# Optimization experiments

Hardware: AMD Instinct MI355X
Metric: run time of the kernel (lower is better)

## Reference

```python
import jax, jax.numpy as jnp
import numpy as np

D = 1024
E = 8
K = 2
NUM_ITER = 2
DT = 0.1
H = 64           # controller_hidden
CTX = 2 * D


def _gelu(t):
    return jax.nn.gelu(t, approximate=False)


def _inl(ctrl, x, v, mu):
    # ctrl: [T, 3D] -> alpha, beta, gate chunks of size D
    alpha_raw, beta_raw, gate_raw = jnp.split(ctrl, 3, axis=-1)
    alpha = jax.nn.sigmoid(alpha_raw)
    beta = jax.nn.softplus(beta_raw)
    gate = jax.nn.sigmoid(gate_raw)
    error = x - mu
    v_next = alpha * v - beta * error
    x_next = x + DT * gate * v_next
    return x_next, v_next


def setup_inputs() -> dict:
    key = jax.random.key(0)
    ks = jax.random.split(key, 20)
    s = 0.02
    inp = {
        'x': jax.random.normal(ks[0], (4, 4096, D), jnp.float32),
        # router MLP
        'w_r1': jax.random.normal(ks[1], (D, D // 4), jnp.float32) * s,
        'b_r1': jnp.zeros((D // 4,), jnp.float32),
        'w_r2': jax.random.normal(ks[2], (D // 4, E), jnp.float32) * s,
        'b_r2': jnp.zeros((E,), jnp.float32),
        # halt gate MLP
        'w_h1': jax.random.normal(ks[3], (D, D // 4), jnp.float32) * s,
        'b_h1': jnp.zeros((D // 4,), jnp.float32),
        'w_h2': jax.random.normal(ks[4], (D // 4, 1), jnp.float32) * s,
        'b_h2': jnp.zeros((1,), jnp.float32),
        # expert tables
        'expert_w1': jax.random.normal(ks[5], (E, CTX, H), jnp.float32) * s,
        'expert_b1': jnp.zeros((E, H), jnp.float32),
        'expert_w2': jax.random.normal(ks[6], (E, H, 3 * D), jnp.float32) * s,
        'expert_b2': jnp.zeros((E, 3 * D), jnp.float32),
        # shared expert
        'w_s1': jax.random.normal(ks[7], (CTX, H), jnp.float32) * s,
        'b_s1': jnp.zeros((H,), jnp.float32),
        'w_s2': jax.random.normal(ks[8], (H, 3 * D), jnp.float32) * s,
        'b_s2': jnp.zeros((3 * D,), jnp.float32),
        'shared_weight': jnp.asarray(0.5, jnp.float32),
        # refine MLP
        'w_f1': jax.random.normal(ks[9], (D, 2 * D), jnp.float32) * s,
        'b_f1': jnp.zeros((2 * D,), jnp.float32),
        'w_f2': jax.random.normal(ks[10], (2 * D, D), jnp.float32) * s,
        'b_f2': jnp.zeros((D,), jnp.float32),
        'integration_weight': jnp.full((D,), 0.5, jnp.float32),
        'mu': jnp.zeros((D,), jnp.float32),
    }
    return inp


def reference(x, w_r1, b_r1, w_r2, b_r2, w_h1, b_h1, w_h2, b_h2,
              expert_w1, expert_b1, expert_w2, expert_b2,
              w_s1, b_s1, w_s2, b_s2, shared_weight,
              w_f1, b_f1, w_f2, b_f2, integration_weight, mu):
    B, N, Dm = x.shape
    xf = x.reshape(B * N, Dm)                       # [T, D]

    # router: top-k over softmax probs, renormalized
    logits = _gelu(xf @ w_r1 + b_r1) @ w_r2 + b_r2  # [T, E]
    probs = jax.nn.softmax(logits, axis=-1)
    top_p, top_i = jax.lax.top_k(probs, K)          # [T, K]
    top_p = top_p / jnp.sum(top_p, axis=-1, keepdims=True)

    flat_idx = top_i.reshape(-1)                    # [T*K]
    flat_w = top_p.reshape(-1, 1)                   # [T*K, 1]

    v = jnp.zeros_like(xf)
    integrated = xf
    for _ in range(NUM_ITER):
        ctx = jnp.concatenate([integrated, v], axis=-1)     # [T, 2D]

        # shared expert path
        shared_ctrl = _gelu(ctx @ w_s1 + b_s1) @ w_s2 + b_s2
        x_shared, v_shared = _inl(shared_ctrl, integrated, v, mu)
        sw = jax.nn.sigmoid(shared_weight)

        # routed experts: gather per-token weights, per-token matvec
        ctx_e = jnp.repeat(ctx, K, axis=0)                  # [T*K, 2D]
        x_e = jnp.repeat(integrated, K, axis=0)
        v_e = jnp.repeat(v, K, axis=0)
        w1 = expert_w1[flat_idx]                            # [T*K, 2D, H]
        b1 = expert_b1[flat_idx]
        w2 = expert_w2[flat_idx]                            # [T*K, H, 3D]
        b2 = expert_b2[flat_idx]
        hidden = _gelu(jnp.einsum('tc,tch->th', ctx_e, w1) + b1)
        ctrl = jnp.einsum('th,tho->to', hidden, w2) + b2    # [T*K, 3D]
        x_r, v_r = _inl(ctrl, x_e, v_e, mu)
        x_r = (x_r * flat_w).reshape(B * N, K, Dm).sum(axis=1)
        v_r = (v_r * flat_w).reshape(B * N, K, Dm).sum(axis=1)

        x_next = sw * x_shared + (1.0 - sw) * x_r
        v_next = sw * v_shared + (1.0 - sw) * v_r

        halt = jax.nn.sigmoid(_gelu(x_next @ w_h1 + b_h1) @ w_h2 + b_h2)  # [T,1]
        refined = _gelu(x_next @ w_f1 + b_f1) @ w_f2 + b_f2               # [T,D]
        integrated = integrated + halt * refined * integration_weight
        v = v_next

    return integrated.reshape(B, N, Dm)
```

## Files before the change

### kernel.cpp

```cpp
#include <hip/hip_runtime.h>


#define TOK   16384
#define DDIM  1024
#define NEXP  8
#define DTC   0.1f
#define NDESC 320
#define GPAD  20480

using f32x4 = __attribute__((ext_vector_type(4))) float;
using bfv8  = __attribute__((ext_vector_type(8))) short;

__device__ __forceinline__ unsigned short f2bf(float x){
  unsigned u = __builtin_bit_cast(unsigned, x);
  u += 0x7fffu + ((u >> 16) & 1u);
  return (unsigned short)(u >> 16);
}
__device__ __forceinline__ float bf2f(unsigned short h){
  return __builtin_bit_cast(float, ((unsigned)h) << 16);
}
__device__ __forceinline__ float sigmf(float x){ return 1.0f/(1.0f+__expf(-x)); }
__device__ __forceinline__ float geluf(float x){
  float u = 1.595769122f * __builtin_fmaf(0.044715f*x*x, x, x);
  return x * sigmf(u);
}
__device__ __forceinline__ float softpf(float x){
  return fmaxf(x, 0.0f) + __logf(1.0f + __expf(-fabsf(x)));
}
__device__ __forceinline__ f32x4 mfma16(bfv8 a, bfv8 b, f32x4 c){
  return __builtin_amdgcn_mfma_f32_16x16x32_bf16(a, b, c, 0, 0, 0);
}
typedef __attribute__((address_space(1))) const void gvoid_t;
typedef __attribute__((address_space(3))) void svoid_t;
__device__ __forceinline__ void gload16(const void* g, void* l){
  __builtin_amdgcn_global_load_lds((gvoid_t*)g, (svoid_t*)l, 16, 0, 0);
}

__global__ __launch_bounds__(256) void transpose_cast(
    const float* __restrict__ src, unsigned short* __restrict__ dst, int R, int C)
{
  __shared__ float tile[32][33];
  size_t bo = (size_t)blockIdx.z * R * C;
  const float* s = src + bo;
  unsigned short* d = dst + bo;
  int c0 = blockIdx.x * 32, r0 = blockIdx.y * 32;
  int tx = threadIdx.x, ty = threadIdx.y;
  #pragma unroll
  for (int j = 0; j < 4; j++)
    tile[ty + 8*j][tx] = s[(size_t)(r0 + ty + 8*j) * C + c0 + tx];
  __syncthreads();
  #pragma unroll
  for (int j = 0; j < 4; j++)
    d[(size_t)(c0 + ty + 8*j) * R + r0 + tx] = f2bf(tile[tx][ty + 8*j]);
}

__global__ __launch_bounds__(256) void xinit_k(
    const float* __restrict__ xf, unsigned short* __restrict__ xb)
{
  const int n = TOK * 256;
  for (int i = blockIdx.x * 256 + threadIdx.x; i < n; i += gridDim.x * 256) {
    float4 f = ((const float4*)xf)[i];
    ushort4 u = {f2bf(f.x), f2bf(f.y), f2bf(f.z), f2bf(f.w)};
    ((ushort4*)xb)[i] = u;
  }
}

__global__ __launch_bounds__(256) void ctxb_k(
    const float* __restrict__ xf, const int* __restrict__ tokmap,
    unsigned short* __restrict__ ctx)
{
  const int g = blockIdx.x, tid = threadIdx.x;
  const int t = tokmap[g];
  if (tid < 128) {
    uint4 o4 = {0,0,0,0};
    if (t >= 0) {
      const float4* s = (const float4*)(xf + (size_t)t * 1024) + tid * 2;
      float4 f0 = s[0], f1 = s[1];
      unsigned short tmp[8] = {f2bf(f0.x), f2bf(f0.y), f2bf(f0.z), f2bf(f0.w),
                               f2bf(f1.x), f2bf(f1.y), f2bf(f1.z), f2bf(f1.w)};
      o4 = *(uint4*)tmp;
    }
    *(uint4*)&ctx[(size_t)g * 2048 + tid * 8] = o4;
  } else {
    *(uint4*)&ctx[(size_t)g * 2048 + 1024 + (tid - 128) * 8] = uint4{0,0,0,0};
  }
}

template<int EPI>
__global__ __launch_bounds__(256) void gemm_k(
    const unsigned short* __restrict__ A, int lda,
    const unsigned short* __restrict__ BT,
    const float* __restrict__ bias, const float* __restrict__ bias2,
    int Kd, int N,
    unsigned short* __restrict__ obf, unsigned short* __restrict__ obf2,
    const float* __restrict__ halt, const float* __restrict__ iw,
    float* __restrict__ integ, unsigned short* __restrict__ ctxX,
    const int* __restrict__ pf)
{
  __shared__ unsigned short As[128][64];
  __shared__ unsigned short Bs[128][64];
  const int total = gridDim.x * gridDim.y;
  const int bid = blockIdx.y * gridDim.x + blockIdx.x;
  const int swz = (bid & 7) * (total >> 3) + (bid >> 3);
  const int bx = swz % gridDim.x, by = swz / gridDim.x;

  const int tid  = threadIdx.x, lane = tid & 63, w = tid >> 6;
  const int wm   = w >> 1, wn = w & 1;
  const int gm0  = by * 128, gn0 = bx * 128;
  const int r8   = lane >> 3;
  const int sseg = (lane & 7) ^ r8;

  const unsigned short* aga[4];
  const unsigned short* bga[4];
  #pragma unroll
  for (int c = 0; c < 4; c++) {
    aga[c] = A  + (size_t)(gm0 + w*32 + c*8 + r8) * lda + sseg*8;
    bga[c] = BT + (size_t)(gn0 + w*32 + c*8 + r8) * Kd  + sseg*8;
  }

  f32x4 acc[4][4];
  #pragma unroll
  for (int i = 0; i < 4; i++)
    #pragma unroll
    for (int j = 0; j < 4; j++)
      acc[i][j] = f32x4{0.f,0.f,0.f,0.f};

  const int xr = (lane & 7) << 3;
  for (int k0 = 0; k0 < Kd; k0 += 64) {
    #pragma unroll
    for (int c = 0; c < 4; c++) gload16(aga[c] + k0, &As[w*32 + c*8][0]);
    #pragma unroll
    for (int c = 0; c < 4; c++) gload16(bga[c] + k0, &Bs[w*32 + c*8][0]);
    __syncthreads();
    #pragma unroll
    for (int kk = 0; kk < 64; kk += 32) {
      const int kof = kk + ((lane >> 4) << 3);
      bfv8 a[4], b[4];
      #pragma unroll
      for (int mf = 0; mf < 4; mf++)
        a[mf] = *(const bfv8*)&As[wm*64 + mf*16 + (lane & 15)][kof ^ xr];
      #pragma unroll
      for (int nf = 0; nf < 4; nf++)
        b[nf] = *(const bfv8*)&Bs[wn*64 + nf*16 + (lane & 15)][kof ^ xr];
      #pragma unroll
      for (int mf = 0; mf < 4; mf++)
        #pragma unroll
        for (int nf = 0; nf < 4; nf++)
          acc[mf][nf] = mfma16(a[mf], b[nf], acc[mf][nf]);
    }
    __syncthreads();
  }

  #pragma unroll
  for (int mf = 0; mf < 4; mf++) {
    #pragma unroll
    for (int nf = 0; nf < 4; nf++) {
      int col = gn0 + wn*64 + nf*16 + (lane & 15);
      float bc;
      if (EPI == 2) bc = (col < 2048) ? bias[col] : bias2[col - 2048];
      else          bc = bias[col];
      #pragma unroll
      for (int r = 0; r < 4; r++) {
        int row = gm0 + wm*64 + mf*16 + ((lane >> 4) << 2) + r;
        float v = acc[mf][nf][r] + bc;
        if (EPI == 0) {
          obf[(size_t)row * N + col] = f2bf(geluf(v));
        } else if (EPI == 2) {
          if (col < 2048) obf [(size_t)row * 2048 + col]         = f2bf(geluf(v));
          else            obf2[(size_t)row * 256 + (col - 2048)] = f2bf(geluf(v));
        } else {
          size_t ix = (size_t)row * DDIM + col;
          float nv = integ[ix] + halt[row] * v * iw[col];
          integ[ix] = nv;
          if (ctxX) ctxX[(size_t)pf[row] * 2048 + col] = f2bf(nv);
        }
      }
    }
  }
}

__global__ __launch_bounds__(256) void router_k(
    const unsigned short* __restrict__ h1, const float* __restrict__ w_r2,
    const float* __restrict__ b_r2, int* __restrict__ topi, float* __restrict__ topw)
{
  int t = blockIdx.x * 4 + (threadIdx.x >> 6);
  int lane = threadIdx.x & 63;
  const unsigned short* hp = h1 + (size_t)t * 256 + lane * 4;
  float hv[4];
  #pragma unroll
  for (int j = 0; j < 4; j++) hv[j] = bf2f(hp[j]);
  float acc[8];
  #pragma unroll
  for (int e = 0; e < 8; e++) acc[e] = 0.f;
  #pragma unroll
  for (int j = 0; j < 4; j++) {
    const float* wr = w_r2 + (size_t)(lane*4 + j) * 8;
    #pragma unroll
    for (int e = 0; e < 8; e++) acc[e] += hv[j] * wr[e];
  }
  #pragma unroll
  for (int off = 32; off > 0; off >>= 1)
    #pragma unroll
    for (int e = 0; e < 8; e++) acc[e] += __shfl_xor(acc[e], off);
  if (lane == 0) {
    float lg[8];
    #pragma unroll
    for (int e = 0; e < 8; e++) lg[e] = acc[e] + b_r2[e];
    int i0 = 0; float m0 = lg[0];
    #pragma unroll
    for (int e = 1; e < 8; e++) if (lg[e] > m0) { m0 = lg[e]; i0 = e; }
    int i1 = -1; float m1 = -3.4e38f;
    #pragma unroll
    for (int e = 0; e < 8; e++) if (e != i0 && lg[e] > m1) { m1 = lg[e]; i1 = e; }
    float w0 = 1.0f / (1.0f + expf(m1 - m0));
    topi[t*2] = i0; topi[t*2+1] = i1;
    topw[t*2] = w0; topw[t*2+1] = 1.0f - w0;
  }
}

__global__ __launch_bounds__(256) void haltgate_k(
    const unsigned short* __restrict__ h1, const float* __restrict__ w_h2,
    const float* __restrict__ b_h2, float* __restrict__ halt)
{
  int t = blockIdx.x * 4 + (threadIdx.x >> 6);
  int lane = threadIdx.x & 63;
  const unsigned short* hp = h1 + (size_t)t * 256 + lane * 4;
  float s = 0.f;
  #pragma unroll
  for (int j = 0; j < 4; j++) s += bf2f(hp[j]) * w_h2[lane*4 + j];
  #pragma unroll
  for (int off = 32; off > 0; off >>= 1) s += __shfl_xor(s, off);
  if (lane == 0) halt[t] = sigmf(s + b_h2[0]);
}

__global__ __launch_bounds__(256) void pairb_k(
    const int* __restrict__ topi, const float* __restrict__ topw,
    int* __restrict__ cnt, int* __restrict__ plist, float* __restrict__ wA)
{
  int t = blockIdx.x * 256 + threadIdx.x;
  int a = topi[2*t], b = topi[2*t+1];
  float wa = topw[2*t];
  if (a > b) { int tmp = a; a = b; b = tmp; wa = 1.0f - wa; }
  int pid = a * 8 + b;
  int pos = atomicAdd(&cnt[pid], 1);
  plist[pid * TOK + pos] = t;
  wA[t] = wa;
}

__global__ void desc_k(const int* __restrict__ cnt, int4* __restrict__ desc,
                       int* __restrict__ ndesc, int* __restrict__ pbase)
{
  if (threadIdx.x == 0 && blockIdx.x == 0) {
    int nt = 0, rb = 0;
    for (int p = 0; p < 64; p++) {
      pbase[p] = rb;
      int c = cnt[p];
      for (int o = 0; o < c; o += 64) {
        int rem = c - o; if (rem > 64) rem = 64;
        desc[nt] = make_int4(p, rb + o, rem, 0);
        nt++;
      }
      rb += (c + 63) & ~63;
    }
    ndesc[0] = nt;
  }
}

__global__ __launch_bounds__(256) void pmap_k(
    const int* __restrict__ cnt, const int* __restrict__ pbase,
    const int* __restrict__ plist, int* __restrict__ tokmap, int* __restrict__ pf)
{
  int pid = blockIdx.x;
  int pos = blockIdx.y * 256 + threadIdx.x;
  if (pos < cnt[pid]) {
    int t = plist[pid * TOK + pos];
    int g = pbase[pid] + pos;
    tokmap[g] = t;
    pf[t] = g;
  }
}

__global__ __launch_bounds__(256) void exp1t_k(
    const unsigned short* __restrict__ ctx,
    const int4* __restrict__ desc, const int* __restrict__ ndesc,
    const unsigned short* __restrict__ ew1T, const float* __restrict__ eb1,
    const unsigned short* __restrict__ ws1T, const float* __restrict__ bs1,
    unsigned short* __restrict__ hiddenG)
{
  __shared__ unsigned short As[64][64];
  __shared__ unsigned short Bs[192][64];
  const int dx = blockIdx.x;
  if (dx >= ndesc[0]) return;
  int4 dd = desc[dx];
  const int pid = dd.x, rbt = dd.y;
  const int e0 = pid >> 3, e1 = pid & 7;
  const unsigned short* w1b[3] = { ew1T + (size_t)e0 * 64 * 2048,
                                   ew1T + (size_t)e1 * 64 * 2048, ws1T };
  const float* b1b[3] = { eb1 + e0 * 64, eb1 + e1 * 64, bs1 };
  const int tid = threadIdx.x, lane = tid & 63, w = tid >> 6;

  const int arow = w*8 + (lane >> 3);
  const int sseg = (lane & 7) ^ (lane >> 3);
  const unsigned short* asrc[2];
  #pragma unroll
  for (int q = 0; q < 2; q++)
    asrc[q] = ctx + (size_t)(rbt + q*32 + arow) * 2048 + sseg * 8;
  const unsigned short* bsrc[3][2];
  #pragma unroll
  for (int p = 0; p < 3; p++)
    #pragma unroll
    for (int q = 0; q < 2; q++)
      bsrc[p][q] = w1b[p] + (size_t)(q*32 + arow) * 2048 + sseg * 8;

  f32x4 acc[3][4];
  #pragma unroll
  for (int p = 0; p < 3; p++)
    #pragma unroll
    for (int j = 0; j < 4; j++)
      acc[p][j] = f32x4{0.f,0.f,0.f,0.f};

  const int xr = (lane & 7) << 3;
  for (int k0 = 0; k0 < 2048; k0 += 64) {
    #pragma unroll
    for (int q = 0; q < 2; q++) gload16(asrc[q] + k0, &As[q*32 + w*8][0]);
    #pragma unroll
    for (int p = 0; p < 3; p++)
      #pragma unroll
      for (int q = 0; q < 2; q++)
        gload16(bsrc[p][q] + k0, &Bs[p*64 + q*32 + w*8][0]);
    __syncthreads();
    #pragma unroll
    for (int kk = 0; kk < 64; kk += 32) {
      const int kof = kk + ((lane >> 4) << 3);
      bfv8 a = *(const bfv8*)&As[w*16 + (lane & 15)][kof ^ xr];
      #pragma unroll
      for (int p = 0; p < 3; p++)
        #pragma unroll
        for (int nf = 0; nf < 4; nf++) {
          bfv8 b = *(const bfv8*)&Bs[p*64 + nf*16 + (lane & 15)][kof ^ xr];
          acc[p][nf] = mfma16(a, b, acc[p][nf]);
        }
    }
    __syncthreads();
  }

  #pragma unroll
  for (int p = 0; p < 3; p++) {
    #pragma unroll
    for (int nf = 0; nf < 4; nf++) {
      int col = nf*16 + (lane & 15);
      float bb = b1b[p][col];
      #pragma unroll
      for (int r = 0; r < 4; r++) {
        int row = w*16 + ((lane >> 4) << 2) + r;
        hiddenG[(size_t)(3*rbt + p*64 + row) * 64 + col] =
            f2bf(geluf(acc[p][nf][r] + bb));
      }
    }
  }
}

__global__ __launch_bounds__(256) void exp2r_k(
    const unsigned short* __restrict__ hiddenG,
    const int4* __restrict__ desc, const int* __restrict__ ndesc,
    const int* __restrict__ tokmap, const float* __restrict__ wA,
    const unsigned short* __restrict__ ew2T, const float* __restrict__ eb2,
    const unsigned short* __restrict__ ws2T, const float* __restrict__ bs2,
    const float* __restrict__ swp, const float* __restrict__ mu,
    unsigned short* __restrict__ ctx, unsigned short* __restrict__ xaccB)
{
  __shared__ unsigned short W2s[2][192][64];
  __shared__ int   s_tok[64];
  __shared__ float s_w[64];
  const int zq = blockIdx.x, dx = blockIdx.y;
  if (dx >= ndesc[0]) return;
  int4 dd = desc[dx];
  const int pid = dd.x, rbt = dd.y, cnt = dd.z;
  const int e0 = pid >> 3, e1 = pid & 7;
  const int tid = threadIdx.x, lane = tid & 63, w = tid >> 6;
  const float sw = sigmf(swp[0]);

  if (tid < 64) {
    int t = tokmap[rbt + tid]; if (t < 0) t = 0;
    s_tok[tid] = t; s_w[tid] = wA[t];
  }

  const unsigned short* w2b[3] = { ew2T + (size_t)e0*3072*64,
                                   ew2T + (size_t)e1*3072*64, ws2T };
  const float* b2b[3] = { eb2 + e0*3072, eb2 + e1*3072, bs2 };
  const int d0q  = zq * 256;
  const int srow = w*8 + (lane >> 3);
  const int sseg = (lane & 7) ^ (lane >> 3);
  const int xr   = (lane & 7) << 3;
  const int cr4  = (lane >> 4) << 2;
  const int arow = w*16 + (lane & 15);
  const int kof8 = (lane >> 4) << 3;

  bfv8 afr[3][2];
  #pragma unroll
  for (int p = 0; p < 3; p++)
    #pragma unroll
    for (int kk = 0; kk < 2; kk++)
      afr[p][kk] = *(const bfv8*)&hiddenG[
          (size_t)(3*rbt + p*64 + arow) * 64 + kk*32 + kof8];

  auto STAGE = [&](int b, int dcq, int path) {
    const int d00 = d0q + dcq*64;
    const unsigned short* w2 = w2b[path];
    #pragma unroll
    for (int q = 0; q < 6; q++) {
      int row  = q*32 + srow;
      int grow = (row >> 6)*1024 + d00 + (row & 63);
      gload16(w2 + (size_t)grow*64 + sseg*8, &W2s[b][q*32 + w*8][0]);
    }
  };

  STAGE(0, 0, 0);
  int toks[4]; float wa4[4];
  float xx[4][4], vv[4][4];

  #pragma unroll
  for (int dcq = 0; dcq < 4; dcq++) {
    const int d00 = d0q + dcq*64;
    f32x4 A4[4], B4[4], C4[4], D4[4];
    #pragma unroll
    for (int cf = 0; cf < 4; cf++) {
      A4[cf] = f32x4{0.f,0.f,0.f,0.f}; B4[cf] = f32x4{0.f,0.f,0.f,0.f};
      C4[cf] = f32x4{0.f,0.f,0.f,0.f}; D4[cf] = f32x4{0.f,0.f,0.f,0.f};
    }
    #pragma unroll
    for (int path = 0; path < 3; path++) {
      const int ph = dcq*3 + path;
      __syncthreads();
      if (ph == 0) {
        #pragma unroll
        for (int r = 0; r < 4; r++) {
          int row = w*16 + cr4 + r;
          toks[r] = s_tok[row]; wa4[r] = s_w[row];
        }
        #pragma unroll
        for (int cf = 0; cf < 4; cf++) {
          int d = d00 + cf*16 + (lane & 15);
          #pragma unroll
          for (int r = 0; r < 4; r++) {
            size_t g = (size_t)(rbt + w*16 + cr4 + r);
            xx[cf][r] = bf2f(ctx[g*2048 + d]);
            vv[cf][r] = bf2f(ctx[g*2048 + 1024 + d]);
          }
        }
      }
      if (ph < 11) {
        const int phn = ph + 1;
        STAGE(phn & 1, phn / 3, phn % 3);
      }
      f32x4 acc[12];
      #pragma unroll
      for (int j = 0; j < 12; j++) acc[j] = f32x4{0.f,0.f,0.f,0.f};
      #pragma unroll
      for (int kk = 0; kk < 2; kk++) {
        const int kof = kk*32 + kof8;
        #pragma unroll
        for (int nf = 0; nf < 12; nf++) {
          bfv8 b = *(const bfv8*)&W2s[ph & 1][nf*16 + (lane & 15)][kof ^ xr];
          acc[nf] = mfma16(afr[path][kk], b, acc[nf]);
        }
      }
      const float* b2 = b2b[path];
      #pragma unroll
      for (int cf = 0; cf < 4; cf++) {
        int d = d00 + cf*16 + (lane & 15);
        float ba = b2[d], bb = b2[1024 + d], bg = b2[2048 + d];
        #pragma unroll
        for (int r = 0; r < 4; r++) {
          float cw = (path == 0) ? (1.f - sw) * wa4[r]
                   : (path == 1) ? (1.f - sw) * (1.f - wa4[r]) : sw;
          float al = sigmf(acc[cf][r] + ba);
          float be = softpf(acc[4 + cf][r] + bb);
          float ga = sigmf(acc[8 + cf][r] + bg);
          A4[cf][r] += cw * al;       B4[cf][r] += cw * be;
          C4[cf][r] += cw * ga * al;  D4[cf][r] += cw * ga * be;
        }
      }
    }
    #pragma unroll
    for (int cf = 0; cf < 4; cf++) {
      int d = d00 + cf*16 + (lane & 15);
      float muv = mu[d];
      #pragma unroll
      for (int r = 0; r < 4; r++) {
        int row = w*16 + cr4 + r;
        size_t g = (size_t)(rbt + row);
        float err = xx[cf][r] - muv;
        float vt = vv[cf][r] * A4[cf][r] - err * B4[cf][r];
        float gv = vv[cf][r] * C4[cf][r] - err * D4[cf][r];
        if (row < cnt) {
          xaccB[(size_t)toks[r]*1024 + d] = f2bf(xx[cf][r] + DTC * gv);
          ctx[g*2048 + 1024 + d]          = f2bf(vt);
        }
      }
    }
    if (dcq < 3) {
      const int dn = d00 + 64;
      #pragma unroll
      for (int cf = 0; cf < 4; cf++) {
        int d = dn + cf*16 + (lane & 15);
        #pragma unroll
        for (int r = 0; r < 4; r++) {
          size_t g = (size_t)(rbt + w*16 + cr4 + r);
          xx[cf][r] = bf2f(ctx[g*2048 + d]);
          vv[cf][r] = bf2f(ctx[g*2048 + 1024 + d]);
        }
      }
    }
  }
}

extern "C" void kernel_launch(void* const* d_in, const int* in_sizes, int n_in,
                              void* d_out, int out_size, void* d_ws, size_t ws_size,
                              hipStream_t stream)
{
  const float* x    = (const float*)d_in[0];
  const float* w_r1 = (const float*)d_in[1];
  const float* b_r1 = (const float*)d_in[2];
  const float* w_r2 = (const float*)d_in[3];
  const float* b_r2 = (const float*)d_in[4];
  const float* w_h1 = (const float*)d_in[5];
  const float* b_h1 = (const float*)d_in[6];
  const float* w_h2 = (const float*)d_in[7];
  const float* b_h2 = (const float*)d_in[8];
  const float* ew1  = (const float*)d_in[9];
  const float* eb1  = (const float*)d_in[10];
  const float* ew2  = (const float*)d_in[11];
  const float* eb2  = (const float*)d_in[12];
  const float* w_s1 = (const float*)d_in[13];
  const float* b_s1 = (const float*)d_in[14];
  const float* w_s2 = (const float*)d_in[15];
  const float* b_s2 = (const float*)d_in[16];
  const float* swt  = (const float*)d_in[17];
  const float* w_f1 = (const float*)d_in[18];
  const float* b_f1 = (const float*)d_in[19];
  const float* w_f2 = (const float*)d_in[20];
  const float* b_f2 = (const float*)d_in[21];
  const float* iw   = (const float*)d_in[22];
  const float* mu   = (const float*)d_in[23];
  float* out = (float*)d_out;

  char* ws = (char*)d_ws;
  size_t off = 0;
  auto take = [&](size_t bytes) -> char* {
    char* p = ws + off;
    off = (off + bytes + 255) & ~(size_t)255;
    return p;
  };
  const size_t TD4 = (size_t)TOK * DDIM * 4;
  unsigned short* xaccB = (unsigned short*)take((size_t)TOK * 1024 * 2);
  unsigned short* ctx   = (unsigned short*)take((size_t)GPAD * 2048 * 2);
  unsigned short* rh    = (unsigned short*)take((size_t)TOK * 2048 * 2);
  unsigned short* hiddenG = (unsigned short*)take((size_t)3 * GPAD * 64 * 2);
  unsigned short* h1 = (unsigned short*)take((size_t)TOK * 256 * 2);
  float* halt = (float*)take((size_t)TOK * 4);
  int*   topi = (int*)take((size_t)TOK * 2 * 4);
  float* topw = (float*)take((size_t)TOK * 2 * 4);
  int*   cnt  = (int*)take(64 * 4);
  int*   ndsc = (int*)take(64);
  int*   pbase= (int*)take(64 * 4);
  int4*  desc = (int4*)take((size_t)NDESC * 16);
  int*   plist= (int*)take((size_t)64 * TOK * 4);
  float* wAa  = (float*)take((size_t)TOK * 4);
  int*   tokmap = (int*)take((size_t)GPAD * 4);
  int*   pf     = (int*)take((size_t)TOK * 4);
  unsigned short* w_r1T = (unsigned short*)take((size_t)256 * 1024 * 2);
  unsigned short* wFH   = (unsigned short*)take((size_t)2304 * 1024 * 2);
  unsigned short* w_f2T = (unsigned short*)take((size_t)1024 * 2048 * 2);
  unsigned short* w_s1T = (unsigned short*)take((size_t)64 * 2048 * 2);
  unsigned short* w_s2T = (unsigned short*)take((size_t)3072 * 64 * 2);
  unsigned short* ew1T  = (unsigned short*)take((size_t)NEXP * 64 * 2048 * 2);
  unsigned short* ew2T  = (unsigned short*)take((size_t)NEXP * 3072 * 64 * 2);
  if (off > ws_size) return;

  hipMemcpyAsync(out, x, TD4, hipMemcpyDeviceToDevice, stream);
  hipMemsetAsync(cnt, 0, 64 * 4, stream);
  hipMemsetAsync(tokmap, 0xFF, (size_t)GPAD * 4, stream);

  dim3 tb(32, 8);
  transpose_cast<<<dim3(  8, 32, 1), tb, 0, stream>>>(w_r1, w_r1T, 1024,  256);
  transpose_cast<<<dim3( 64, 32, 1), tb, 0, stream>>>(w_f1, wFH, 1024, 2048);
  transpose_cast<<<dim3(  8, 32, 1), tb, 0, stream>>>(w_h1, wFH + (size_t)2048*1024, 1024, 256);
  transpose_cast<<<dim3( 32, 64, 1), tb, 0, stream>>>(w_f2, w_f2T, 2048, 1024);
  transpose_cast<<<dim3(  2, 64, 1), tb, 0, stream>>>(w_s1, w_s1T, 2048,   64);
  transpose_cast<<<dim3( 96,  2, 1), tb, 0, stream>>>(w_s2, w_s2T,   64, 3072);
  transpose_cast<<<dim3(  2, 64, 8), tb, 0, stream>>>(ew1,  ew1T,  2048,   64);
  transpose_cast<<<dim3( 96,  2, 8), tb, 0, stream>>>(ew2,  ew2T,    64, 3072);

  xinit_k<<<2048, 256, 0, stream>>>(x, xaccB);
  gemm_k<0><<<dim3(2, 128), 256, 0, stream>>>(
      xaccB, 1024, w_r1T, b_r1, nullptr, 1024, 256, h1, nullptr,
      nullptr, nullptr, nullptr, nullptr, nullptr);
  router_k<<<TOK / 4, 256, 0, stream>>>(h1, w_r2, b_r2, topi, topw);
  pairb_k<<<TOK / 256, 256, 0, stream>>>(topi, topw, cnt, plist, wAa);
  desc_k<<<1, 64, 0, stream>>>(cnt, desc, ndsc, pbase);
  pmap_k<<<dim3(64, 64), 256, 0, stream>>>(cnt, pbase, plist, tokmap, pf);
  ctxb_k<<<GPAD, 256, 0, stream>>>(out, tokmap, ctx);

  for (int it = 0; it < 2; it++) {
    exp1t_k<<<NDESC, 256, 0, stream>>>(ctx, desc, ndsc,
                                       ew1T, eb1, w_s1T, b_s1, hiddenG);
    exp2r_k<<<dim3(4, NDESC), 256, 0, stream>>>(
        hiddenG, desc, ndsc, tokmap, wAa, ew2T, eb2, w_s2T, b_s2,
        swt, mu, ctx, xaccB);
    gemm_k<2><<<dim3(18, 128), 256, 0, stream>>>(
        xaccB, 1024, wFH, b_f1, b_h1, 1024, 2304, rh, h1,
        nullptr, nullptr, nullptr, nullptr, nullptr);
    haltgate_k<<<TOK / 4, 256, 0, stream>>>(h1, w_h2, b_h2, halt);
    gemm_k<1><<<dim3(8, 128), 256, 0, stream>>>(
        rh, 2048, w_f2T, b_f2, nullptr, 2048, 1024, nullptr, nullptr,
        halt, iw, out, (it == 0) ? ctx : nullptr, pf);
  }
}
```

Baseline: 1.324 ms.

## Split expert layer-1 across paths and cut register pressure in expert layer-2

The first expert kernel now launches one block per (path, descriptor) instead of computing all three paths (two routed experts plus shared) in one block. This triples the grid and shrinks the shared-memory B tile and accumulator set. The second expert kernel processes the three gate outputs in two halves of columns and folds the INL update into running vt/gv accumulators instead of four coefficient sums. It also sets a launch bound of 3 blocks per SM, all to lower register use and raise occupancy. In exchange, the context tile is re-read once per path, and the tighter launch bound may cause spills.

```diff
diff --git a/kernel.cpp b/kernel.cpp
--- a/kernel.cpp
+++ b/kernel.cpp
@@ -280,7 +280,7 @@
   }
 }
 
-__global__ __launch_bounds__(256) void exp1t_k(
+__global__ __launch_bounds__(256) void exp1p_k(
     const unsigned short* __restrict__ ctx,
     const int4* __restrict__ desc, const int* __restrict__ ndesc,
     const unsigned short* __restrict__ ew1T, const float* __restrict__ eb1,
@@ -288,79 +288,64 @@
     unsigned short* __restrict__ hiddenG)
 {
   __shared__ unsigned short As[64][64];
-  __shared__ unsigned short Bs[192][64];
-  const int dx = blockIdx.x;
+  __shared__ unsigned short Bs[64][64];
+  const int path = blockIdx.x, dx = blockIdx.y;
   if (dx >= ndesc[0]) return;
   int4 dd = desc[dx];
   const int pid = dd.x, rbt = dd.y;
-  const int e0 = pid >> 3, e1 = pid & 7;
-  const unsigned short* w1b[3] = { ew1T + (size_t)e0 * 64 * 2048,
-                                   ew1T + (size_t)e1 * 64 * 2048, ws1T };
-  const float* b1b[3] = { eb1 + e0 * 64, eb1 + e1 * 64, bs1 };
+  const int ep = (path == 0) ? (pid >> 3) : (pid & 7);
+  const unsigned short* w1 = (path < 2) ? ew1T + (size_t)ep * 64 * 2048 : ws1T;
+  const float* b1 = (path < 2) ? eb1 + ep * 64 : bs1;
   const int tid = threadIdx.x, lane = tid & 63, w = tid >> 6;
 
   const int arow = w*8 + (lane >> 3);
   const int sseg = (lane & 7) ^ (lane >> 3);
   const unsigned short* asrc[2];
-  #pragma unroll
-  for (int q = 0; q < 2; q++)
+  const unsigned short* bsrc[2];
+  #pragma unroll
+  for (int q = 0; q < 2; q++) {
     asrc[q] = ctx + (size_t)(rbt + q*32 + arow) * 2048 + sseg * 8;
-  const unsigned short* bsrc[3][2];
-  #pragma unroll
-  for (int p = 0; p < 3; p++)
-    #pragma unroll
-    for (int q = 0; q < 2; q++)
-      bsrc[p][q] = w1b[p] + (size_t)(q*32 + arow) * 2048 + sseg * 8;
-
-  f32x4 acc[3][4];
-  #pragma unroll
-  for (int p = 0; p < 3; p++)
-    #pragma unroll
-    for (int j = 0; j < 4; j++)
-      acc[p][j] = f32x4{0.f,0.f,0.f,0.f};
+    bsrc[q] = w1  + (size_t)(q*32 + arow) * 2048 + sseg * 8;
+  }
+
+  f32x4 acc[4];
+  #pragma unroll
+  for (int j = 0; j < 4; j++) acc[j] = f32x4{0.f,0.f,0.f,0.f};
 
   const int xr = (lane & 7) << 3;
   for (int k0 = 0; k0 < 2048; k0 += 64) {
     #pragma unroll
     for (int q = 0; q < 2; q++) gload16(asrc[q] + k0, &As[q*32 + w*8][0]);
     #pragma unroll
-    for (int p = 0; p < 3; p++)
-      #pragma unroll
-      for (int q = 0; q < 2; q++)
-        gload16(bsrc[p][q] + k0, &Bs[p*64 + q*32 + w*8][0]);
+    for (int q = 0; q < 2; q++) gload16(bsrc[q] + k0, &Bs[q*32 + w*8][0]);
     __syncthreads();
     #pragma unroll
     for (int kk = 0; kk < 64; kk += 32) {
       const int kof = kk + ((lane >> 4) << 3);
       bfv8 a = *(const bfv8*)&As[w*16 + (lane & 15)][kof ^ xr];
       #pragma unroll
-      for (int p = 0; p < 3; p++)
-        #pragma unroll
-        for (int nf = 0; nf < 4; nf++) {
-          bfv8 b = *(const bfv8*)&Bs[p*64 + nf*16 + (lane & 15)][kof ^ xr];
-          acc[p][nf] = mfma16(a, b, acc[p][nf]);
-        }
+      for (int nf = 0; nf < 4; nf++) {
+        bfv8 b = *(const bfv8*)&Bs[nf*16 + (lane & 15)][kof ^ xr];
+        acc[nf] = mfma16(a, b, acc[nf]);
+      }
     }
     __syncthreads();
   }
 
   #pragma unroll
-  for (int p = 0; p < 3; p++) {
-    #pragma unroll
-    for (int nf = 0; nf < 4; nf++) {
-      int col = nf*16 + (lane & 15);
-      float bb = b1b[p][col];
-      #pragma unroll
-      for (int r = 0; r < 4; r++) {
-        int row = w*16 + ((lane >> 4) << 2) + r;
-        hiddenG[(size_t)(3*rbt + p*64 + row) * 64 + col] =
-            f2bf(geluf(acc[p][nf][r] + bb));
-      }
-    }
-  }
-}
-
-__global__ __launch_bounds__(256) void exp2r_k(
+  for (int nf = 0; nf < 4; nf++) {
+    int col = nf*16 + (lane & 15);
+    float bb = b1[col];
+    #pragma unroll
+    for (int r = 0; r < 4; r++) {
+      int row = w*16 + ((lane >> 4) << 2) + r;
+      hiddenG[(size_t)(3*rbt + path*64 + row) * 64 + col] =
+          f2bf(geluf(acc[nf][r] + bb));
+    }
+  }
+}
+
+__global__ __launch_bounds__(256, 3) void exp2r_k(
     const unsigned short* __restrict__ hiddenG,
     const int4* __restrict__ desc, const int* __restrict__ ndesc,
     const int* __restrict__ tokmap, const float* __restrict__ wA,
@@ -378,7 +363,8 @@
   const int pid = dd.x, rbt = dd.y, cnt = dd.z;
   const int e0 = pid >> 3, e1 = pid & 7;
   const int tid = threadIdx.x, lane = tid & 63, w = tid >> 6;
-  const float sw = sigmf(swp[0]);
+  const float sw  = sigmf(swp[0]);
+  const float swc = 1.0f - sw;
 
   if (tid < 64) {
     int t = tokmap[rbt + tid]; if (t < 0) t = 0;
@@ -416,36 +402,34 @@
   };
 
   STAGE(0, 0, 0);
-  int toks[4]; float wa4[4];
-  float xx[4][4], vv[4][4];
+  float wa4p[4];
+  float err[4][4], vv[4][4], muv4[4];
+  float vt[4][4], gv[4][4];
 
   #pragma unroll
   for (int dcq = 0; dcq < 4; dcq++) {
     const int d00 = d0q + dcq*64;
-    f32x4 A4[4], B4[4], C4[4], D4[4];
-    #pragma unroll
-    for (int cf = 0; cf < 4; cf++) {
-      A4[cf] = f32x4{0.f,0.f,0.f,0.f}; B4[cf] = f32x4{0.f,0.f,0.f,0.f};
-      C4[cf] = f32x4{0.f,0.f,0.f,0.f}; D4[cf] = f32x4{0.f,0.f,0.f,0.f};
-    }
+    #pragma unroll
+    for (int cf = 0; cf < 4; cf++)
+      #pragma unroll
+      for (int r = 0; r < 4; r++) { vt[cf][r] = 0.f; gv[cf][r] = 0.f; }
     #pragma unroll
     for (int path = 0; path < 3; path++) {
       const int ph = dcq*3 + path;
       __syncthreads();
       if (ph == 0) {
         #pragma unroll
-        for (int r = 0; r < 4; r++) {
-          int row = w*16 + cr4 + r;
-          toks[r] = s_tok[row]; wa4[r] = s_w[row];
-        }
+        for (int r = 0; r < 4; r++)
+          wa4p[r] = swc * s_w[w*16 + cr4 + r];
         #pragma unroll
         for (int cf = 0; cf < 4; cf++) {
           int d = d00 + cf*16 + (lane & 15);
+          muv4[cf] = mu[d];
           #pragma unroll
           for (int r = 0; r < 4; r++) {
             size_t g = (size_t)(rbt + w*16 + cr4 + r);
-            xx[cf][r] = bf2f(ctx[g*2048 + d]);
-            vv[cf][r] = bf2f(ctx[g*2048 + 1024 + d]);
+            err[cf][r] = bf2f(ctx[g*2048 + d]) - muv4[cf];
+            vv[cf][r]  = bf2f(ctx[g*2048 + 1024 + d]);
           }
         }
       }
@@ -453,49 +437,53 @@
         const int phn = ph + 1;
         STAGE(phn & 1, phn / 3, phn % 3);
       }
-      f32x4 acc[12];
-      #pragma unroll
-      for (int j = 0; j < 12; j++) acc[j] = f32x4{0.f,0.f,0.f,0.f};
-      #pragma unroll
-      for (int kk = 0; kk < 2; kk++) {
-        const int kof = kk*32 + kof8;
+      const float* b2 = b2b[path];
+      #pragma unroll
+      for (int cfh = 0; cfh < 2; cfh++) {
+        f32x4 acc[6];
         #pragma unroll
-        for (int nf = 0; nf < 12; nf++) {
-          bfv8 b = *(const bfv8*)&W2s[ph & 1][nf*16 + (lane & 15)][kof ^ xr];
-          acc[nf] = mfma16(afr[path][kk], b, acc[nf]);
+        for (int j = 0; j < 6; j++) acc[j] = f32x4{0.f,0.f,0.f,0.f};
+        #pragma unroll
+        for (int kk = 0; kk < 2; kk++) {
+          const int kof = kk*32 + kof8;
+          #pragma unroll
+          for (int j = 0; j < 6; j++) {
+            int nf = cfh*2 + (j & 1) + (j >> 1) * 4;
+            bfv8 b = *(const bfv8*)&W2s[ph & 1][nf*16 + (lane & 15)][kof ^ xr];
+            acc[j] = mfma16(afr[path][kk], b, acc[j]);
+          }
         }
-      }
-      const float* b2 = b2b[path];
-      #pragma unroll
-      for (int cf = 0; cf < 4; cf++) {
-        int d = d00 + cf*16 + (lane & 15);
-        float ba = b2[d], bb = b2[1024 + d], bg = b2[2048 + d];
         #pragma unroll
-        for (int r = 0; r < 4; r++) {
-          float cw = (path == 0) ? (1.f - sw) * wa4[r]
-                   : (path == 1) ? (1.f - sw) * (1.f - wa4[r]) : sw;
-          float al = sigmf(acc[cf][r] + ba);
-          float be = softpf(acc[4 + cf][r] + bb);
-          float ga = sigmf(acc[8 + cf][r] + bg);
-          A4[cf][r] += cw * al;       B4[cf][r] += cw * be;
-          C4[cf][r] += cw * ga * al;  D4[cf][r] += cw * ga * be;
+        for (int cj = 0; cj < 2; cj++) {
+          int cf = cfh*2 + cj;
+          int d = d00 + cf*16 + (lane & 15);
+          float ba = b2[d], bb = b2[1024 + d], bg = b2[2048 + d];
+          #pragma unroll
+          for (int r = 0; r < 4; r++) {
+            float cw = (path == 0) ? wa4p[r]
+                     : (path == 1) ? (swc - wa4p[r]) : sw;
+            float al = sigmf(acc[cj][r] + ba);
+            float be = softpf(acc[2 + cj][r] + bb);
+            float ga = sigmf(acc[4 + cj][r] + bg);
+            float vn = al * vv[cf][r] - be * err[cf][r];
+            vt[cf][r] = __builtin_fmaf(cw, vn, vt[cf][r]);
+            gv[cf][r] = __builtin_fmaf(cw, ga * vn, gv[cf][r]);
+          }
         }
       }
     }
     #pragma unroll
     for (int cf = 0; cf < 4; cf++) {
       int d = d00 + cf*16 + (lane & 15);
-      float muv = mu[d];
       #pragma unroll
       for (int r = 0; r < 4; r++) {
         int row = w*16 + cr4 + r;
         size_t g = (size_t)(rbt + row);
-        float err = xx[cf][r] - muv;
-        float vt = vv[cf][r] * A4[cf][r] - err * B4[cf][r];
-        float gv = vv[cf][r] * C4[cf][r] - err * D4[cf][r];
+        float xx = err[cf][r] + muv4[cf];
         if (row < cnt) {
-          xaccB[(size_t)toks[r]*1024 + d] = f2bf(xx[cf][r] + DTC * gv);
-          ctx[g*2048 + 1024 + d]          = f2bf(vt);
+          int tok = s_tok[row];
+          xaccB[(size_t)tok*1024 + d] = f2bf(xx + DTC * gv[cf][r]);
+          ctx[g*2048 + 1024 + d]      = f2bf(vt[cf][r]);
         }
       }
     }
@@ -504,11 +492,12 @@
       #pragma unroll
       for (int cf = 0; cf < 4; cf++) {
         int d = dn + cf*16 + (lane & 15);
+        muv4[cf] = mu[d];
         #pragma unroll
         for (int r = 0; r < 4; r++) {
           size_t g = (size_t)(rbt + w*16 + cr4 + r);
-          xx[cf][r] = bf2f(ctx[g*2048 + d]);
-          vv[cf][r] = bf2f(ctx[g*2048 + 1024 + d]);
+          err[cf][r] = bf2f(ctx[g*2048 + d]) - muv4[cf];
+          vv[cf][r]  = bf2f(ctx[g*2048 + 1024 + d]);
         }
       }
     }
@@ -603,8 +592,8 @@
   ctxb_k<<<GPAD, 256, 0, stream>>>(out, tokmap, ctx);
 
   for (int it = 0; it < 2; it++) {
-    exp1t_k<<<NDESC, 256, 0, stream>>>(ctx, desc, ndsc,
-                                       ew1T, eb1, w_s1T, b_s1, hiddenG);
+    exp1p_k<<<dim3(3, NDESC), 256, 0, stream>>>(
+        ctx, desc, ndsc, ew1T, eb1, w_s1T, b_s1, hiddenG);
     exp2r_k<<<dim3(4, NDESC), 256, 0, stream>>>(
         hiddenG, desc, ndsc, tokmap, wAa, ew2T, eb2, w_s2T, b_s2,
         swt, mu, ctx, xaccB);
```

Result: slower. 2.332 ms (+76.2%).
